# Optimization experiments

Hardware: AMD Instinct MI355X
Metric: run time of the kernel (lower is better)

## Reference

```python
import jax, jax.numpy as jnp
import numpy as np


def setup_inputs() -> dict:
    key = jax.random.key(0)
    k1, k2, k3, k4 = jax.random.split(key, 4)
    N, C_in, C_out, H, W, K = 32, 128, 256, 56, 56, 3
    x = jax.random.normal(k1, (N, C_in, H, W), dtype=jnp.float32)
    # ternary weights in {-1, 0, +1}, stored as int8 like the torch buffer
    w_q = jax.random.randint(k2, (C_out, C_in, K, K), -1, 2).astype(jnp.int8)
    s = jax.random.uniform(k3, (C_out, 1, 1), dtype=jnp.float32) + 0.5
    bias = jax.random.normal(k4, (C_out,), dtype=jnp.float32)
    return {"x": x, "w_q": w_q, "s": s, "bias": bias}


def reference(x, w_q, s, bias):
    # y = conv2d(x, w_q.float()) * s + bias, stride=1, padding=1, dilation=1, groups=1
    w = w_q.astype(x.dtype)  # ternary {-1,0,+1} cast to float, as in torch
    y = jax.lax.conv_general_dilated(
        x, w,
        window_strides=(1, 1),
        padding=((1, 1), (1, 1)),
        lhs_dilation=(1, 1),
        rhs_dilation=(1, 1),
        dimension_numbers=("NCHW", "OIHW", "NCHW"),
        feature_group_count=1,
    )
    y = y * s  # s: [C_out,1,1] broadcasts over [N,C_out,H,W]
    y = y + bias.reshape(1, -1, 1, 1)
    return y
```

## Files before the change

### kernel.cpp

```cpp
#include <hip/hip_runtime.h>
#include <hip/hip_bf16.h>

typedef unsigned short ushort_t;

#define N_IMG 32
#define C_IN  128
#define C_OUT 256
#define H_SZ  56
#define W_SZ  56
#define HW_SZ (H_SZ * W_SZ)
#define K_TOT (C_IN * 9)
#define WP 64
#define HP 58
#define ROW_E (WP * C_IN)

typedef __attribute__((ext_vector_type(8))) short bf16x8;
typedef __attribute__((ext_vector_type(4))) float floatx4;

__device__ __forceinline__ void gl_lds16(const ushort_t* g, ushort_t* l) {
  __builtin_amdgcn_global_load_lds(
      (const __attribute__((address_space(1))) void*)g,
      (__attribute__((address_space(3))) void*)l, 16, 0, 0);
}

__device__ __forceinline__ ushort_t f2bf(float f) {
  __hip_bfloat16 b = __float2bfloat16(f);
  return *reinterpret_cast<ushort_t*>(&b);
}

__global__ void wtrans_kernel(const int* __restrict__ wq, ushort_t* __restrict__ wt) {
  int idx = blockIdx.x * 256 + threadIdx.x;
  if (idx >= C_OUT * K_TOT) return;
  int co = idx / K_TOT;
  int k  = idx - co * K_TOT;
  int tap = k >> 7;
  int c   = k & 127;
  int kh = tap / 3, kw = tap - kh * 3;
  int v = wq[((co * C_IN + c) * 3 + kh) * 3 + kw];
  wt[idx] = f2bf((float)v);
}

__global__ __launch_bounds__(256) void xpad_kernel(const float* __restrict__ x,
                                                   ushort_t* __restrict__ xp) {
  int b = blockIdx.x;
  int t = threadIdx.x;
  ushort_t* row = xp + (size_t)b * ROW_E;
  int n = b / HP;
  int h1 = b - n * HP;
  if (b >= N_IMG * HP || h1 == 0 || h1 == HP - 1) {
    uint4 z = {0u, 0u, 0u, 0u};
    uint4* r4 = (uint4*)row;
#pragma unroll
    for (int i = 0; i < 4; ++i) r4[i * 256 + t] = z;
    return;
  }
  __shared__ float tile[C_IN * 57];
  int h = h1 - 1;
  const float* xb = x + (size_t)n * C_IN * HW_SZ + h * W_SZ;
#pragma unroll
  for (int i = 0; i < 7; ++i) {
    int idx = i * 256 + t;
    int c = idx / 14, f = idx - c * 14;
    float4 v = *(const float4*)(xb + (size_t)c * HW_SZ + f * 4);
    float* dst = &tile[c * 57 + f * 4];
    dst[0] = v.x; dst[1] = v.y; dst[2] = v.z; dst[3] = v.w;
  }
  __syncthreads();
  unsigned int* r32 = (unsigned int*)row;
#pragma unroll
  for (int i = 0; i < 16; ++i) {
    int idx = i * 256 + t;
    int wp = idx >> 6, cp = idx & 63;
    unsigned int u = 0;
    if (wp >= 1 && wp <= W_SZ) {
      int w = wp - 1;
      u = (unsigned int)f2bf(tile[(2 * cp) * 57 + w]) |
          ((unsigned int)f2bf(tile[(2 * cp + 1) * 57 + w]) << 16);
    }
    r32[wp * 64 + cp] = u;
  }
}

__global__ __launch_bounds__(256) void bitconv_kernel(
    const ushort_t* __restrict__ wt, const ushort_t* __restrict__ xp,
    const float* __restrict__ s, const float* __restrict__ bias,
    float* __restrict__ out) {
  __shared__ ushort_t As[128 * 32];
  __shared__ ushort_t Bs[128 * 32];

  int d = blockIdx.x;
  int xcd = d & 7;
  int r   = d >> 3;
  int co0 = (r & 1) * 128;
  int sp_tile = xcd * 112 + (r >> 1);
  int nh0 = sp_tile * 2;
  int n  = nh0 / H_SZ;
  int hh = nh0 - n * H_SZ;

  int tid  = threadIdx.x;
  int lane = tid & 63;
  int wid  = tid >> 6;
  int l15  = lane & 15;
  int quad = lane >> 4;
  int wave_m = (wid >> 1) * 64;
  int wave_n = (wid & 1) * 64;
  int lrow = lane >> 2;
  int lchk = (lane & 3) * 8;

  const ushort_t* a_src[2];
  const ushort_t* b_src[2];
  ushort_t* a_dst[2];
  ushort_t* b_dst[2];
#pragma unroll
  for (int g = 0; g < 2; ++g) {
    int rrow = wid * 32 + g * 16 + lrow;
    a_src[g] = wt + (size_t)(co0 + rrow) * K_TOT + lchk;
    int hrow = rrow >> 6, wpp = (rrow & 63) + 1;
    b_src[g] = xp + (size_t)((n * HP + hh + 1 + hrow) * WP + wpp) * C_IN + lchk;
    a_dst[g] = &As[(wid * 32 + g * 16) * 32];
    b_dst[g] = &Bs[(wid * 32 + g * 16) * 32];
  }

  floatx4 acc[4][4];
#pragma unroll
  for (int mi = 0; mi < 4; ++mi)
#pragma unroll
    for (int ni = 0; ni < 4; ++ni)
      acc[mi][ni] = (floatx4){0.f, 0.f, 0.f, 0.f};

  for (int tap = 0; tap < 9; ++tap) {
    int dh = tap / 3 - 1;
    int dw = tap - (dh + 1) * 3 - 1;
    int boff = dh * (WP * C_IN) + dw * C_IN;
    int aoff = tap * C_IN;
#pragma unroll
    for (int c0 = 0; c0 < C_IN; c0 += 32) {
#pragma unroll
      for (int g = 0; g < 2; ++g) {
        gl_lds16(a_src[g] + aoff + c0, a_dst[g]);
        gl_lds16(b_src[g] + boff + c0, b_dst[g]);
      }
      __syncthreads();
      bf16x8 af[4], bfv[4];
#pragma unroll
      for (int mi = 0; mi < 4; ++mi)
        af[mi] = *(const bf16x8*)&As[(wave_m + mi * 16 + l15) * 32 + quad * 8];
#pragma unroll
      for (int ni = 0; ni < 4; ++ni)
        bfv[ni] = *(const bf16x8*)&Bs[(wave_n + ni * 16 + l15) * 32 + quad * 8];
#pragma unroll
      for (int mi = 0; mi < 4; ++mi)
#pragma unroll
        for (int ni = 0; ni < 4; ++ni)
          acc[mi][ni] = __builtin_amdgcn_mfma_f32_16x16x32_bf16(
              af[mi], bfv[ni], acc[mi][ni], 0, 0, 0);
      __syncthreads();
    }
  }

  int h_out = hh + (wid & 1);
#pragma unroll
  for (int mi = 0; mi < 4; ++mi) {
#pragma unroll
    for (int rg = 0; rg < 4; ++rg) {
      int co = co0 + wave_m + mi * 16 + quad * 4 + rg;
      float sv = s[co];
      float bv = bias[co];
      float* ob = out + (size_t)(n * C_OUT + co) * HW_SZ + h_out * W_SZ;
#pragma unroll
      for (int ni = 0; ni < 4; ++ni) {
        int wpp = ni * 16 + l15;
        if (wpp < W_SZ)
          ob[wpp] = acc[mi][ni][rg] * sv + bv;
      }
    }
  }
}

extern "C" void kernel_launch(void* const* d_in, const int* in_sizes, int n_in,
                              void* d_out, int out_size, void* d_ws, size_t ws_size,
                              hipStream_t stream) {
  const float* x    = (const float*)d_in[0];
  const int*   wq   = (const int*)d_in[1];
  const float* s    = (const float*)d_in[2];
  const float* bias = (const float*)d_in[3];
  float* out = (float*)d_out;

  char* ws = (char*)d_ws;
  ushort_t* wt = (ushort_t*)ws;
  ushort_t* xp = (ushort_t*)(ws + 589824);

  hipLaunchKernelGGL(wtrans_kernel, dim3((C_OUT * K_TOT) / 256), dim3(256), 0, stream,
                     wq, wt);
  hipLaunchKernelGGL(xpad_kernel, dim3(N_IMG * HP + 1), dim3(256), 0, stream, x, xp);
  hipLaunchKernelGGL(bitconv_kernel, dim3(1792), dim3(256), 0, stream,
                     wt, xp, s, bias, out);
}
```

Measured before the change: 227.1 us.

## Double-buffer LDS tiles in bitconv with prefetch of next K-stage

Turns the single LDS buffer for the A and B tiles into two buffers and flattens the tap/channel loops into 36 stages. Each iteration issues the global-to-LDS loads for the next stage before computing on the current one, and waits only on the older loads with vmcnt(4). The goal is to hide global load latency behind MFMA work. LDS use per block doubles, which may reduce occupancy, and correctness depends on the hand-written waitcnt and barriers; the loop also no longer issues an lgkmcnt wait before the barrier after the LDS reads.

```diff
diff --git a/kernel.cpp b/kernel.cpp
--- a/kernel.cpp
+++ b/kernel.cpp
@@ -85,8 +85,8 @@
     const ushort_t* __restrict__ wt, const ushort_t* __restrict__ xp,
     const float* __restrict__ s, const float* __restrict__ bias,
     float* __restrict__ out) {
-  __shared__ ushort_t As[128 * 32];
-  __shared__ ushort_t Bs[128 * 32];
+  __shared__ ushort_t As[2][128 * 32];
+  __shared__ ushort_t Bs[2][128 * 32];
 
   int d = blockIdx.x;
   int xcd = d & 7;
@@ -109,16 +109,14 @@
 
   const ushort_t* a_src[2];
   const ushort_t* b_src[2];
-  ushort_t* a_dst[2];
-  ushort_t* b_dst[2];
+  int dst_off[2];
 #pragma unroll
   for (int g = 0; g < 2; ++g) {
     int rrow = wid * 32 + g * 16 + lrow;
     a_src[g] = wt + (size_t)(co0 + rrow) * K_TOT + lchk;
     int hrow = rrow >> 6, wpp = (rrow & 63) + 1;
     b_src[g] = xp + (size_t)((n * HP + hh + 1 + hrow) * WP + wpp) * C_IN + lchk;
-    a_dst[g] = &As[(wid * 32 + g * 16) * 32];
-    b_dst[g] = &Bs[(wid * 32 + g * 16) * 32];
+    dst_off[g] = (wid * 32 + g * 16) * 32;
   }
 
   floatx4 acc[4][4];
@@ -128,34 +126,47 @@
     for (int ni = 0; ni < 4; ++ni)
       acc[mi][ni] = (floatx4){0.f, 0.f, 0.f, 0.f};
 
-  for (int tap = 0; tap < 9; ++tap) {
-    int dh = tap / 3 - 1;
-    int dw = tap - (dh + 1) * 3 - 1;
-    int boff = dh * (WP * C_IN) + dw * C_IN;
-    int aoff = tap * C_IN;
-#pragma unroll
-    for (int c0 = 0; c0 < C_IN; c0 += 32) {
-#pragma unroll
-      for (int g = 0; g < 2; ++g) {
-        gl_lds16(a_src[g] + aoff + c0, a_dst[g]);
-        gl_lds16(b_src[g] + boff + c0, b_dst[g]);
-      }
-      __syncthreads();
-      bf16x8 af[4], bfv[4];
-#pragma unroll
-      for (int mi = 0; mi < 4; ++mi)
-        af[mi] = *(const bf16x8*)&As[(wave_m + mi * 16 + l15) * 32 + quad * 8];
+  auto stage = [&](int st, int buf) {
+    int tap = st >> 2;
+    int c0  = (st & 3) << 5;
+    int kh  = tap / 3;
+    int kw  = tap - kh * 3;
+    int aoff = tap * C_IN + c0;
+    int boff = (kh - 1) * ROW_E + (kw - 1) * C_IN + c0;
+#pragma unroll
+    for (int g = 0; g < 2; ++g) {
+      gl_lds16(a_src[g] + aoff, &As[buf][dst_off[g]]);
+      gl_lds16(b_src[g] + boff, &Bs[buf][dst_off[g]]);
+    }
+  };
+
+  stage(0, 0);
+  int cur = 0;
+  for (int st = 0; st < 36; ++st) {
+    if (st < 35) {
+      stage(st + 1, cur ^ 1);
+      asm volatile("s_waitcnt vmcnt(4)" ::: "memory");
+    } else {
+      asm volatile("s_waitcnt vmcnt(0)" ::: "memory");
+    }
+    __builtin_amdgcn_s_barrier();
+
+    bf16x8 af[4], bfv[4];
+#pragma unroll
+    for (int mi = 0; mi < 4; ++mi)
+      af[mi] = *(const bf16x8*)&As[cur][(wave_m + mi * 16 + l15) * 32 + quad * 8];
+#pragma unroll
+    for (int ni = 0; ni < 4; ++ni)
+      bfv[ni] = *(const bf16x8*)&Bs[cur][(wave_n + ni * 16 + l15) * 32 + quad * 8];
+#pragma unroll
+    for (int mi = 0; mi < 4; ++mi)
 #pragma unroll
       for (int ni = 0; ni < 4; ++ni)
-        bfv[ni] = *(const bf16x8*)&Bs[(wave_n + ni * 16 + l15) * 32 + quad * 8];
-#pragma unroll
-      for (int mi = 0; mi < 4; ++mi)
-#pragma unroll
-        for (int ni = 0; ni < 4; ++ni)
-          acc[mi][ni] = __builtin_amdgcn_mfma_f32_16x16x32_bf16(
-              af[mi], bfv[ni], acc[mi][ni], 0, 0, 0);
-      __syncthreads();
-    }
+        acc[mi][ni] = __builtin_amdgcn_mfma_f32_16x16x32_bf16(
+            af[mi], bfv[ni], acc[mi][ni], 0, 0, 0);
+
+    __builtin_amdgcn_s_barrier();
+    cur ^= 1;
   }
 
   int h_out = hh + (wid & 1);
```

New measurement: 236.9 us. 1.04x slower.
